# Performance work log

Hardware: AMD Instinct MI355X
Metric: run time of the kernel (lower is better)

Reference implementation:

```python
import jax, jax.numpy as jnp
import numpy as np

H = 256
V = 50257
L = 2048
B = 32


def setup_inputs() -> dict:
    key = jax.random.key(0)
    ks = jax.random.split(key, 14)
    s = 0.05  # weight scale
    return {
        "tokens": jax.random.randint(ks[0], (B,), 0, V),
        "hidden": jax.random.normal(ks[1], (1, B, H), jnp.float32),
        "cell": jax.random.normal(ks[2], (1, B, H), jnp.float32),
        "encoder_outputs": jax.random.normal(ks[3], (B, L, H), jnp.float32),
        "emb_table": jax.random.normal(ks[4], (V, H), jnp.float32) * s,
        "W_attn": jax.random.normal(ks[5], (H, 2 * H), jnp.float32) * s,
        "b_attn": jax.random.normal(ks[6], (H,), jnp.float32) * s,
        "v": jax.random.normal(ks[7], (H,), jnp.float32) * s,
        "W_ih": jax.random.normal(ks[8], (4 * H, 2 * H), jnp.float32) * s,
        "b_ih": jax.random.normal(ks[9], (4 * H,), jnp.float32) * s,
        "W_hh": jax.random.normal(ks[10], (4 * H, H), jnp.float32) * s,
        "b_hh": jax.random.normal(ks[11], (4 * H,), jnp.float32) * s,
        "W_out": jax.random.normal(ks[12], (V, 2 * H), jnp.float32) * s,
        "b_out": jax.random.normal(ks[13], (V,), jnp.float32) * s,
    }


def reference(tokens, hidden, cell, encoder_outputs, emb_table, W_attn, b_attn, v,
              W_ih, b_ih, W_hh, b_hh, W_out, b_out):
    # embedded: (B, H); dropout is identity in eval mode
    embedded = emb_table[tokens]
    h_last = hidden[-1]  # (B, H)

    # Bahdanau-style energy: attn(cat(h, e)) then dot with v (NO tanh, per source)
    # split the 2H-input linear into hidden part and encoder part
    Wh, We = W_attn[:, :H], W_attn[:, H:]
    eh = h_last @ Wh.T                                      # (B, H)
    ee = jnp.einsum('blh,kh->blk', encoder_outputs, We)     # (B, L, H)
    energy = eh[:, None, :] + ee + b_attn                   # (B, L, H)
    scores = energy @ v                                     # (B, L)
    attn_weights = jax.nn.softmax(scores, axis=-1)          # (B, L)

    # context = bmm(attn_weights, encoder_outputs)
    attn_applied = jnp.einsum('bl,blh->bh', attn_weights, encoder_outputs)  # (B, H)

    # single-step LSTM, input = cat(embedded, context): (B, 2H)
    x = jnp.concatenate([embedded, attn_applied], axis=-1)
    gates = x @ W_ih.T + b_ih + hidden[0] @ W_hh.T + b_hh   # (B, 4H)
    i_g, f_g, g_g, o_g = jnp.split(gates, 4, axis=-1)
    c_new = jax.nn.sigmoid(f_g) * cell[0] + jax.nn.sigmoid(i_g) * jnp.tanh(g_g)
    h_new = jax.nn.sigmoid(o_g) * jnp.tanh(c_new)           # (B, H)

    # output projection on cat(lstm_out, context): (B, 2H) -> (B, V)
    logits = jnp.concatenate([h_new, attn_applied], axis=-1) @ W_out.T + b_out
    log_probs = jax.nn.log_softmax(logits, axis=-1)

    return (log_probs, h_new[None], c_new[None], attn_weights[:, None, :])
```

## Files before the change

kernel.cpp:

```cpp
#include <hip/hip_runtime.h>
#include <cstddef>

#define H   256
#define L   2048
#define B   32
#define V   50257
#define H2  512
#define H4  1024
#define CH  64
#define NCH (L/CH)

#define LP_OFF 0
#define HN_OFF (B*V)
#define CN_OFF (HN_OFF + B*H)
#define AW_OFF (CN_OFF + B*H)

#define WS_WP    0
#define WS_XG    (WS_WP + 32*256)
#define WS_XL    (WS_XG + B*H2)
#define WS_S     (WS_XL + B*H2)
#define WS_AV    (WS_S + B*L)
#define WS_AM    (WS_AV + B*NCH*H)
#define WS_AZ    (WS_AM + B*NCH)
#define WS_GATES (WS_AZ + B*NCH)
#define WS_PM    (WS_GATES + B*H4)
#define WS_PZ    (WS_PM + 12800)
#define WS_M     (WS_PZ + 12800)
#define WS_LZ    (WS_M + 32)

#define NBLK_LOG 393

typedef __attribute__((ext_vector_type(8))) short bf16x8;
typedef __attribute__((ext_vector_type(4))) float f32x4;

__device__ inline unsigned short f2bf(float f) {
    unsigned u = __builtin_bit_cast(unsigned, f);
    u += 0x7FFFu + ((u >> 16) & 1u);
    return (unsigned short)(u >> 16);
}

__global__ __launch_bounds__(256) void k_prep(const float* __restrict__ W_attn,
                                              const float* __restrict__ v,
                                              float* __restrict__ ws) {
    int p = blockIdx.x, t = threadIdx.x;
    const float* base = W_attn + H + t;
    float acc = 0.f;
    #pragma unroll
    for (int kk = 0; kk < 8; kk++) {
        int k = p * 8 + kk;
        acc += v[k] * base[(size_t)k * H2];
    }
    ws[WS_WP + p * 256 + t] = acc;
}

__global__ __launch_bounds__(256) void k_attn_flash(const float* __restrict__ enc,
                                                    float* __restrict__ ws) {
    int bid = blockIdx.x;
    int b = bid >> 5, chunk = bid & (NCH - 1);
    int t = threadIdx.x;
    int wave = t >> 6, lane = t & 63;
    int g = lane >> 4, u = lane & 15;
    __shared__ float w_s[256];
    __shared__ float s_lds[CH];
    __shared__ float p_lds[CH];
    __shared__ float red[CH];
    __shared__ float vec_lds[4][256];

    float wsum = 0.f;
    #pragma unroll 8
    for (int p = 0; p < 32; p++) wsum += ws[WS_WP + p * 256 + t];
    w_s[t] = wsum;
    __syncthreads();

    size_t rowbase = (size_t)b * L + chunk * CH;
    const float4* w4s = (const float4*)w_s;
    float4 w0 = w4s[u], w1 = w4s[16 + u], w2 = w4s[32 + u], w3 = w4s[48 + u];

    #pragma unroll
    for (int ir = 0; ir < 4; ir++) {
        int rl = wave * 16 + ir * 4 + g;
        const float4* e4 = (const float4*)(enc + (rowbase + rl) * H);
        float4 a0 = e4[u], a1 = e4[16 + u], a2 = e4[32 + u], a3 = e4[48 + u];
        float p = a0.x * w0.x + a0.y * w0.y + a0.z * w0.z + a0.w * w0.w
                + a1.x * w1.x + a1.y * w1.y + a1.z * w1.z + a1.w * w1.w
                + a2.x * w2.x + a2.y * w2.y + a2.z * w2.z + a2.w * w2.w
                + a3.x * w3.x + a3.y * w3.y + a3.z * w3.z + a3.w * w3.w;
        p += __shfl_down(p, 8); p += __shfl_down(p, 4);
        p += __shfl_down(p, 2); p += __shfl_down(p, 1);
        if (u == 0) s_lds[rl] = p;
    }
    __syncthreads();

    if (t < CH) red[t] = s_lds[t];
    __syncthreads();
    for (int off = 32; off; off >>= 1) { if (t < off) red[t] = fmaxf(red[t], red[t + off]); __syncthreads(); }
    float m = red[0];
    __syncthreads();
    if (t < CH) {
        float e = __expf(s_lds[t] - m);
        p_lds[t] = e; red[t] = e;
        ws[WS_S + rowbase + t] = s_lds[t];
    }
    __syncthreads();
    for (int off = 32; off; off >>= 1) { if (t < off) red[t] += red[t + off]; __syncthreads(); }

    float4 acc = make_float4(0.f, 0.f, 0.f, 0.f);
    const float4* ebase = (const float4*)(enc + (rowbase + wave * 16) * H);
    #pragma unroll 4
    for (int i = 0; i < 16; i++) {
        float p = p_lds[wave * 16 + i];
        float4 a = ebase[i * 64 + lane];
        acc.x += p * a.x; acc.y += p * a.y; acc.z += p * a.z; acc.w += p * a.w;
    }
    *(float4*)&vec_lds[wave][lane * 4] = acc;
    __syncthreads();
    ws[WS_AV + (size_t)bid * 256 + t] = vec_lds[0][t] + vec_lds[1][t] + vec_lds[2][t] + vec_lds[3][t];
    if (t == 0) { ws[WS_AM + bid] = m; ws[WS_AZ + bid] = red[0]; }
}

__global__ __launch_bounds__(256) void k_attn_comb(const int* __restrict__ tokens,
                                                   const float* __restrict__ emb,
                                                   float* __restrict__ ws,
                                                   float* __restrict__ out) {
    int b = blockIdx.x, t = threadIdx.x;
    __shared__ float mc[NCH], zc[NCH];
    if (t < NCH) { mc[t] = ws[WS_AM + b * NCH + t]; zc[t] = ws[WS_AZ + b * NCH + t]; }
    __syncthreads();
    float M = -1e30f;
    #pragma unroll
    for (int c = 0; c < NCH; c++) M = fmaxf(M, mc[c]);
    float Z = 0.f;
    #pragma unroll
    for (int c = 0; c < NCH; c++) Z += zc[c] * __expf(mc[c] - M);
    float inv = 1.f / Z;
    float acc = 0.f;
    #pragma unroll 8
    for (int c = 0; c < NCH; c++) acc += __expf(mc[c] - M) * ws[WS_AV + (size_t)(b * NCH + c) * 256 + t];
    acc *= inv;
    ws[WS_XG + b * H2 + H + t] = acc;
    ws[WS_XL + b * H2 + H + t] = acc;
    int tok = tokens[b];
    ws[WS_XG + b * H2 + t] = emb[(size_t)tok * H + t];
    #pragma unroll
    for (int j = 0; j < 8; j++) {
        int l = t + 256 * j;
        out[AW_OFF + (size_t)b * L + l] = __expf(ws[WS_S + (size_t)b * L + l] - M) * inv;
    }
}

__global__ __launch_bounds__(256) void k_gates(const float* __restrict__ W_ih, const float* __restrict__ b_ih,
                                               const float* __restrict__ W_hh, const float* __restrict__ b_hh,
                                               const float* __restrict__ hidden, float* __restrict__ ws) {
    int t = threadIdx.x;
    int wave = t >> 6, lane = t & 63;
    int o = blockIdx.x * 4 + wave;
    int b = o >> 10, j = o & 1023;
    const float4* wi = (const float4*)(W_ih + (size_t)j * H2);
    const float4* xg = (const float4*)(ws + WS_XG + (size_t)b * H2);
    float4 a0 = wi[lane * 2], a1 = wi[lane * 2 + 1];
    float4 x0 = xg[lane * 2], x1 = xg[lane * 2 + 1];
    float p = a0.x * x0.x + a0.y * x0.y + a0.z * x0.z + a0.w * x0.w
            + a1.x * x1.x + a1.y * x1.y + a1.z * x1.z + a1.w * x1.w;
    const float4* wh = (const float4*)(W_hh + (size_t)j * H);
    const float4* hp = (const float4*)(hidden + (size_t)b * H);
    float4 a2 = wh[lane], x2 = hp[lane];
    p += a2.x * x2.x + a2.y * x2.y + a2.z * x2.z + a2.w * x2.w;
    #pragma unroll
    for (int off = 32; off; off >>= 1) p += __shfl_down(p, off);
    if (lane == 0) ws[WS_GATES + o] = p + b_ih[j] + b_hh[j];
}

__global__ __launch_bounds__(256) void k_lstm(const float* __restrict__ cell,
                                              float* __restrict__ ws, float* __restrict__ out) {
    int b = blockIdx.x, t = threadIdx.x;
    const float* g = ws + WS_GATES + (size_t)b * H4;
    float ig = g[t], fg = g[H + t], gg = g[2 * H + t], og = g[3 * H + t];
    float c = cell[(size_t)b * H + t];
    float si = 1.f / (1.f + expf(-ig));
    float sf = 1.f / (1.f + expf(-fg));
    float so = 1.f / (1.f + expf(-og));
    float cn = sf * c + si * tanhf(gg);
    float hn = so * tanhf(cn);
    out[HN_OFF + b * H + t] = hn;
    out[CN_OFF + b * H + t] = cn;
    ws[WS_XL + b * H2 + t] = hn;
}

__global__ __launch_bounds__(256) void k_logits(const float* __restrict__ W_out,
                                                const float* __restrict__ b_out,
                                                float* __restrict__ ws,
                                                float* __restrict__ out) {
    __shared__ unsigned short Xl[32 * 520];
    int t = threadIdx.x;
    const float4* xl4 = (const float4*)(ws + WS_XL);
    #pragma unroll
    for (int it = 0; it < 16; it++) {
        int fi = t + 256 * it;
        int b = fi >> 7, kq = fi & 127;
        float4 xv = xl4[b * 128 + kq];
        unsigned p0 = (unsigned)f2bf(xv.x) | ((unsigned)f2bf(xv.y) << 16);
        unsigned p1 = (unsigned)f2bf(xv.z) | ((unsigned)f2bf(xv.w) << 16);
        unsigned* dst = (unsigned*)&Xl[b * 520 + kq * 4];
        dst[0] = p0; dst[1] = p1;
    }
    __syncthreads();

    int wave = t >> 6, lane = t & 63, quad = lane >> 4, m = lane & 15;
    int rbase = blockIdx.x * 128 + wave * 32;
    f32x4 zero4 = {0.f, 0.f, 0.f, 0.f};
    f32x4 acc[2][2];
    acc[0][0] = zero4; acc[0][1] = zero4; acc[1][0] = zero4; acc[1][1] = zero4;

    int r0 = rbase + m;
    int r1 = rbase + 16 + m;
    bool v0 = r0 < V, v1 = r1 < V;
    const float* wp0 = W_out + (size_t)r0 * H2 + quad * 8;
    const float* wp1 = W_out + (size_t)r1 * H2 + quad * 8;

    for (int kp = 0; kp < 16; kp++) {
        int k0 = kp * 32;
        bf16x8 a0 = {0,0,0,0,0,0,0,0}, a1 = {0,0,0,0,0,0,0,0};
        if (v0) {
            float4 lo = *(const float4*)(wp0 + k0);
            float4 hi = *(const float4*)(wp0 + k0 + 4);
            a0[0]=(short)f2bf(lo.x); a0[1]=(short)f2bf(lo.y); a0[2]=(short)f2bf(lo.z); a0[3]=(short)f2bf(lo.w);
            a0[4]=(short)f2bf(hi.x); a0[5]=(short)f2bf(hi.y); a0[6]=(short)f2bf(hi.z); a0[7]=(short)f2bf(hi.w);
        }
        if (v1) {
            float4 lo = *(const float4*)(wp1 + k0);
            float4 hi = *(const float4*)(wp1 + k0 + 4);
            a1[0]=(short)f2bf(lo.x); a1[1]=(short)f2bf(lo.y); a1[2]=(short)f2bf(lo.z); a1[3]=(short)f2bf(lo.w);
            a1[4]=(short)f2bf(hi.x); a1[5]=(short)f2bf(hi.y); a1[6]=(short)f2bf(hi.z); a1[7]=(short)f2bf(hi.w);
        }
        bf16x8 b0 = *(bf16x8*)&Xl[(size_t)m * 520 + k0 + quad * 8];
        bf16x8 b1 = *(bf16x8*)&Xl[(size_t)(16 + m) * 520 + k0 + quad * 8];
        acc[0][0] = __builtin_amdgcn_mfma_f32_16x16x32_bf16(a0, b0, acc[0][0], 0, 0, 0);
        acc[0][1] = __builtin_amdgcn_mfma_f32_16x16x32_bf16(a0, b1, acc[0][1], 0, 0, 0);
        acc[1][0] = __builtin_amdgcn_mfma_f32_16x16x32_bf16(a1, b0, acc[1][0], 0, 0, 0);
        acc[1][1] = __builtin_amdgcn_mfma_f32_16x16x32_bf16(a1, b1, acc[1][1], 0, 0, 0);
    }

    float val[2][2][4];
    #pragma unroll
    for (int s = 0; s < 2; s++) {
        #pragma unroll
        for (int i = 0; i < 4; i++) {
            int rr = rbase + s * 16 + quad * 4 + i;
            float bo = (rr < V) ? b_out[rr] : 0.f;
            #pragma unroll
            for (int nt = 0; nt < 2; nt++) {
                float vv = acc[s][nt][i] + bo;
                if (rr < V) {
                    int bcol = nt * 16 + m;
                    out[(size_t)bcol * V + rr] = vv;
                    val[s][nt][i] = vv;
                } else {
                    val[s][nt][i] = -1e30f;
                }
            }
        }
    }
    float pm[2], pz[2];
    #pragma unroll
    for (int nt = 0; nt < 2; nt++) {
        float mx = -1e30f;
        #pragma unroll
        for (int s = 0; s < 2; s++)
            #pragma unroll
            for (int i = 0; i < 4; i++) mx = fmaxf(mx, val[s][nt][i]);
        float sm = 0.f;
        #pragma unroll
        for (int s = 0; s < 2; s++)
            #pragma unroll
            for (int i = 0; i < 4; i++) sm += __expf(val[s][nt][i] - mx);
        pm[nt] = mx; pz[nt] = sm;
    }
    #pragma unroll
    for (int off = 16; off <= 32; off <<= 1) {
        #pragma unroll
        for (int nt = 0; nt < 2; nt++) {
            float om = __shfl_xor(pm[nt], off);
            float oz = __shfl_xor(pz[nt], off);
            float nm = fmaxf(pm[nt], om);
            pz[nt] = pz[nt] * __expf(pm[nt] - nm) + oz * __expf(om - nm);
            pm[nt] = nm;
        }
    }
    __syncthreads();
    float* red = (float*)Xl;
    if (quad == 0) {
        #pragma unroll
        for (int nt = 0; nt < 2; nt++) {
            red[wave * 32 + nt * 16 + m]       = pm[nt];
            red[128 + wave * 32 + nt * 16 + m] = pz[nt];
        }
    }
    __syncthreads();
    if (t < 32) {
        float mf = -1e30f;
        #pragma unroll
        for (int w = 0; w < 4; w++) mf = fmaxf(mf, red[w * 32 + t]);
        float z = 0.f;
        #pragma unroll
        for (int w = 0; w < 4; w++) z += red[128 + w * 32 + t] * __expf(red[w * 32 + t] - mf);
        ws[WS_PM + t * 400 + blockIdx.x] = mf;
        ws[WS_PZ + t * 400 + blockIdx.x] = z;
    }
}

__global__ __launch_bounds__(256) void k_lsm_comb(float* __restrict__ ws) {
    int b = blockIdx.x, t = threadIdx.x;
    float m = -1e30f, z = 0.f;
    for (int i = t; i < NBLK_LOG; i += 256) {
        float mi = ws[WS_PM + b * 400 + i];
        float zi = ws[WS_PZ + b * 400 + i];
        float nm = fmaxf(m, mi);
        z = z * __expf(m - nm) + zi * __expf(mi - nm);
        m = nm;
    }
    __shared__ float rm[256], rz[256];
    rm[t] = m; rz[t] = z; __syncthreads();
    for (int off = 128; off; off >>= 1) {
        if (t < off) {
            float m2 = rm[t + off], z2 = rz[t + off];
            float nm = fmaxf(rm[t], m2);
            rz[t] = rz[t] * __expf(rm[t] - nm) + z2 * __expf(m2 - nm);
            rm[t] = nm;
        }
        __syncthreads();
    }
    if (t == 0) { ws[WS_M + b] = rm[0]; ws[WS_LZ + b] = logf(rz[0]); }
}

__global__ __launch_bounds__(256) void k_lsm_final(const float* __restrict__ ws, float* __restrict__ out) {
    int b = blockIdx.y;
    int r = blockIdx.x * 256 + threadIdx.x;
    if (r < V) {
        size_t i = (size_t)b * V + r;
        out[i] = out[i] - ws[WS_M + b] - ws[WS_LZ + b];
    }
}

extern "C" void kernel_launch(void* const* d_in, const int* in_sizes, int n_in,
                              void* d_out, int out_size, void* d_ws, size_t ws_size,
                              hipStream_t stream) {
    const int*   tokens = (const int*)d_in[0];
    const float* hidden = (const float*)d_in[1];
    const float* cell   = (const float*)d_in[2];
    const float* enc    = (const float*)d_in[3];
    const float* emb    = (const float*)d_in[4];
    const float* W_attn = (const float*)d_in[5];
    const float* v      = (const float*)d_in[7];
    const float* W_ih   = (const float*)d_in[8];
    const float* b_ih   = (const float*)d_in[9];
    const float* W_hh   = (const float*)d_in[10];
    const float* b_hh   = (const float*)d_in[11];
    const float* W_out  = (const float*)d_in[12];
    const float* b_out  = (const float*)d_in[13];
    float* out = (float*)d_out;
    float* ws  = (float*)d_ws;

    k_prep<<<32, 256, 0, stream>>>(W_attn, v, ws);
    k_attn_flash<<<B * NCH, 256, 0, stream>>>(enc, ws);
    k_attn_comb<<<B, 256, 0, stream>>>(tokens, emb, ws, out);
    k_gates<<<(B * H4) / 4, 256, 0, stream>>>(W_ih, b_ih, W_hh, b_hh, hidden, ws);
    k_lstm<<<B, 256, 0, stream>>>(cell, ws, out);
    k_logits<<<NBLK_LOG, 256, 0, stream>>>(W_out, b_out, ws, out);
    k_lsm_comb<<<B, 256, 0, stream>>>(ws);
    k_lsm_final<<<dim3((V + 255) / 256, B), 256, 0, stream>>>(ws, out);
}
```

Measured before the change: 290.1 us.

## Fuse attention combine, LSTM gates and cell update; merge log-softmax reduction into final pass

Attention-combine, gate GEMV and LSTM cell kernels become a single kernel with 128 blocks, one per batch and hidden quarter. Each block keeps the context and embedding vectors in LDS and computes the four gates for its 64 hidden units before applying the LSTM update. The separate log-softmax combine kernel is folded into the final kernel, so every block redundantly reduces the 393 partial max/sum values. This saves several launches and workspace round trips, but each block recomputes the attention combine and the gate GEMV runs on far fewer blocks.

```diff
diff --git a/kernel.cpp b/kernel.cpp
--- a/kernel.cpp
+++ b/kernel.cpp
@@ -16,17 +16,13 @@
 #define AW_OFF (CN_OFF + B*H)
 
 #define WS_WP    0
-#define WS_XG    (WS_WP + 32*256)
-#define WS_XL    (WS_XG + B*H2)
+#define WS_XL    (WS_WP + 32*256)
 #define WS_S     (WS_XL + B*H2)
 #define WS_AV    (WS_S + B*L)
 #define WS_AM    (WS_AV + B*NCH*H)
 #define WS_AZ    (WS_AM + B*NCH)
-#define WS_GATES (WS_AZ + B*NCH)
-#define WS_PM    (WS_GATES + B*H4)
+#define WS_PM    (WS_AZ + B*NCH)
 #define WS_PZ    (WS_PM + 12800)
-#define WS_M     (WS_PZ + 12800)
-#define WS_LZ    (WS_M + 32)
 
 #define NBLK_LOG 393
 
@@ -118,12 +114,22 @@
     if (t == 0) { ws[WS_AM + bid] = m; ws[WS_AZ + bid] = red[0]; }
 }
 
-__global__ __launch_bounds__(256) void k_attn_comb(const int* __restrict__ tokens,
-                                                   const float* __restrict__ emb,
-                                                   float* __restrict__ ws,
-                                                   float* __restrict__ out) {
-    int b = blockIdx.x, t = threadIdx.x;
+__global__ __launch_bounds__(256) void k_mid(const int* __restrict__ tokens,
+                                             const float* __restrict__ emb,
+                                             const float* __restrict__ hidden,
+                                             const float* __restrict__ cell,
+                                             const float* __restrict__ W_ih, const float* __restrict__ b_ih,
+                                             const float* __restrict__ W_hh, const float* __restrict__ b_hh,
+                                             float* __restrict__ ws,
+                                             float* __restrict__ out) {
+    int bid = blockIdx.x;
+    int b = bid >> 2, hg = bid & 3;
+    int t = threadIdx.x;
     __shared__ float mc[NCH], zc[NCH];
+    __shared__ float x_s[H2];
+    __shared__ float h_s[H];
+    __shared__ float gl[4][64];
+
     if (t < NCH) { mc[t] = ws[WS_AM + b * NCH + t]; zc[t] = ws[WS_AZ + b * NCH + t]; }
     __syncthreads();
     float M = -1e30f;
@@ -137,53 +143,61 @@
     #pragma unroll 8
     for (int c = 0; c < NCH; c++) acc += __expf(mc[c] - M) * ws[WS_AV + (size_t)(b * NCH + c) * 256 + t];
     acc *= inv;
-    ws[WS_XG + b * H2 + H + t] = acc;
-    ws[WS_XL + b * H2 + H + t] = acc;
+    x_s[H + t] = acc;
     int tok = tokens[b];
-    ws[WS_XG + b * H2 + t] = emb[(size_t)tok * H + t];
-    #pragma unroll
-    for (int j = 0; j < 8; j++) {
-        int l = t + 256 * j;
-        out[AW_OFF + (size_t)b * L + l] = __expf(ws[WS_S + (size_t)b * L + l] - M) * inv;
-    }
-}
-
-__global__ __launch_bounds__(256) void k_gates(const float* __restrict__ W_ih, const float* __restrict__ b_ih,
-                                               const float* __restrict__ W_hh, const float* __restrict__ b_hh,
-                                               const float* __restrict__ hidden, float* __restrict__ ws) {
-    int t = threadIdx.x;
-    int wave = t >> 6, lane = t & 63;
-    int o = blockIdx.x * 4 + wave;
-    int b = o >> 10, j = o & 1023;
-    const float4* wi = (const float4*)(W_ih + (size_t)j * H2);
-    const float4* xg = (const float4*)(ws + WS_XG + (size_t)b * H2);
-    float4 a0 = wi[lane * 2], a1 = wi[lane * 2 + 1];
-    float4 x0 = xg[lane * 2], x1 = xg[lane * 2 + 1];
-    float p = a0.x * x0.x + a0.y * x0.y + a0.z * x0.z + a0.w * x0.w
-            + a1.x * x1.x + a1.y * x1.y + a1.z * x1.z + a1.w * x1.w;
-    const float4* wh = (const float4*)(W_hh + (size_t)j * H);
-    const float4* hp = (const float4*)(hidden + (size_t)b * H);
-    float4 a2 = wh[lane], x2 = hp[lane];
-    p += a2.x * x2.x + a2.y * x2.y + a2.z * x2.z + a2.w * x2.w;
-    #pragma unroll
-    for (int off = 32; off; off >>= 1) p += __shfl_down(p, off);
-    if (lane == 0) ws[WS_GATES + o] = p + b_ih[j] + b_hh[j];
-}
-
-__global__ __launch_bounds__(256) void k_lstm(const float* __restrict__ cell,
-                                              float* __restrict__ ws, float* __restrict__ out) {
-    int b = blockIdx.x, t = threadIdx.x;
-    const float* g = ws + WS_GATES + (size_t)b * H4;
-    float ig = g[t], fg = g[H + t], gg = g[2 * H + t], og = g[3 * H + t];
-    float c = cell[(size_t)b * H + t];
-    float si = 1.f / (1.f + expf(-ig));
-    float sf = 1.f / (1.f + expf(-fg));
-    float so = 1.f / (1.f + expf(-og));
-    float cn = sf * c + si * tanhf(gg);
-    float hn = so * tanhf(cn);
-    out[HN_OFF + b * H + t] = hn;
-    out[CN_OFF + b * H + t] = cn;
-    ws[WS_XL + b * H2 + t] = hn;
+    x_s[t] = emb[(size_t)tok * H + t];
+    h_s[t] = hidden[(size_t)b * H + t];
+    if (hg == 0) {
+        ws[WS_XL + b * H2 + H + t] = acc;
+        #pragma unroll
+        for (int j = 0; j < 8; j++) {
+            int l = t + 256 * j;
+            out[AW_OFF + (size_t)b * L + l] = __expf(ws[WS_S + (size_t)b * L + l] - M) * inv;
+        }
+    }
+    __syncthreads();
+
+    int wave = t >> 6, lane = t & 63, g = lane >> 4, u = lane & 15;
+    const float4* xs4 = (const float4*)x_s;
+    const float4* hs4 = (const float4*)h_s;
+    #pragma unroll 2
+    for (int ir = 0; ir < 16; ir++) {
+        int e = hg * 64 + ir * 4 + g;
+        int j = wave * 256 + e;
+        const float4* wi = (const float4*)(W_ih + (size_t)j * H2);
+        const float4* wh = (const float4*)(W_hh + (size_t)j * H);
+        float p = 0.f;
+        #pragma unroll
+        for (int q = 0; q < 8; q++) {
+            float4 a = wi[u + 16 * q];
+            float4 x = xs4[u + 16 * q];
+            p += a.x * x.x + a.y * x.y + a.z * x.z + a.w * x.w;
+        }
+        #pragma unroll
+        for (int q = 0; q < 4; q++) {
+            float4 a = wh[u + 16 * q];
+            float4 x = hs4[u + 16 * q];
+            p += a.x * x.x + a.y * x.y + a.z * x.z + a.w * x.w;
+        }
+        p += __shfl_down(p, 8); p += __shfl_down(p, 4);
+        p += __shfl_down(p, 2); p += __shfl_down(p, 1);
+        if (u == 0) gl[wave][ir * 4 + g] = p + b_ih[j] + b_hh[j];
+    }
+    __syncthreads();
+
+    if (t < 64) {
+        int h = hg * 64 + t;
+        float ig = gl[0][t], fg = gl[1][t], gg = gl[2][t], og = gl[3][t];
+        float c = cell[(size_t)b * H + h];
+        float si = 1.f / (1.f + __expf(-ig));
+        float sf = 1.f / (1.f + __expf(-fg));
+        float so = 1.f / (1.f + __expf(-og));
+        float cn = sf * c + si * tanhf(gg);
+        float hn = so * tanhf(cn);
+        out[HN_OFF + (size_t)b * H + h] = hn;
+        out[CN_OFF + (size_t)b * H + h] = cn;
+        ws[WS_XL + b * H2 + h] = hn;
+    }
 }
 
 __global__ __launch_bounds__(256) void k_logits(const float* __restrict__ W_out,
@@ -308,8 +322,9 @@
     }
 }
 
-__global__ __launch_bounds__(256) void k_lsm_comb(float* __restrict__ ws) {
-    int b = blockIdx.x, t = threadIdx.x;
+__global__ __launch_bounds__(256) void k_lsm_final(const float* __restrict__ ws,
+                                                   float* __restrict__ out) {
+    int b = blockIdx.y, t = threadIdx.x;
     float m = -1e30f, z = 0.f;
     for (int i = t; i < NBLK_LOG; i += 256) {
         float mi = ws[WS_PM + b * 400 + i];
@@ -329,15 +344,11 @@
         }
         __syncthreads();
     }
-    if (t == 0) { ws[WS_M + b] = rm[0]; ws[WS_LZ + b] = logf(rz[0]); }
-}
-
-__global__ __launch_bounds__(256) void k_lsm_final(const float* __restrict__ ws, float* __restrict__ out) {
-    int b = blockIdx.y;
-    int r = blockIdx.x * 256 + threadIdx.x;
+    float sub = rm[0] + logf(rz[0]);
+    int r = blockIdx.x * 256 + t;
     if (r < V) {
         size_t i = (size_t)b * V + r;
-        out[i] = out[i] - ws[WS_M + b] - ws[WS_LZ + b];
+        out[i] = out[i] - sub;
     }
 }
 
@@ -362,10 +373,8 @@
 
     k_prep<<<32, 256, 0, stream>>>(W_attn, v, ws);
     k_attn_flash<<<B * NCH, 256, 0, stream>>>(enc, ws);
-    k_attn_comb<<<B, 256, 0, stream>>>(tokens, emb, ws, out);
-    k_gates<<<(B * H4) / 4, 256, 0, stream>>>(W_ih, b_ih, W_hh, b_hh, hidden, ws);
-    k_lstm<<<B, 256, 0, stream>>>(cell, ws, out);
+    k_mid<<<B * 4, 256, 0, stream>>>(tokens, emb, hidden, cell,
+                                     W_ih, b_ih, W_hh, b_hh, ws, out);
     k_logits<<<NBLK_LOG, 256, 0, stream>>>(W_out, b_out, ws, out);
-    k_lsm_comb<<<B, 256, 0, stream>>>(ws);
     k_lsm_final<<<dim3((V + 255) / 256, B), 256, 0, stream>>>(ws, out);
 }
```

After: 297.1 us. 1.02x slower.
